# Performance work log

Hardware: AMD Instinct MI355X
Metric: run time of the kernel (lower is better)

Reference implementation:

```python
import jax, jax.numpy as jnp
import numpy as np

H = 1024          # rnn hidden dim
D = H // 2        # coarse/fine half
E = H // 8        # embed dim = 128
COND = H // 2     # conditioning (upsampled mel) dim = 512
EPS = 1e-5
TILE = 16


def _bn(x, scale, offset):
    # haiku BatchNorm, training mode: batch stats over (N, L)
    mean = jnp.mean(x, axis=(0, 1), keepdims=True)
    var = jnp.mean(jnp.square(x), axis=(0, 1), keepdims=True) - jnp.square(mean)
    return scale * (x - mean) * jax.lax.rsqrt(var + EPS) + offset


def _conv(x, w, rate=1):
    return jax.lax.conv_general_dilated(
        x, w, window_strides=(1,), padding='VALID', rhs_dilation=(rate,),
        dimension_numbers=('NWC', 'WIO', 'NWC'))


def _up(x, w, stride):
    # Conv1DTranspose with kernel 1, SAME padding: scatter x@w to positions i*stride
    N, L, _ = x.shape
    y = jnp.einsum('nlc,cd->nld', x, w)
    out = jnp.zeros((N, L, stride, y.shape[-1]), y.dtype).at[:, :, 0, :].set(y)
    return out.reshape(N, L * stride, y.shape[-1])


def _iw_mask():
    m = jnp.ones((COND + 3 * E, 3 * H), jnp.float32)
    for j in (0, 2, 4):  # coarse_t embed cannot see coarse half of u, r, e gates
        m = m.at[-E:, j * D:(j + 1) * D].set(0.0)
    return m


def _forward(x, mel, conv_in_w, bn0_s, bn0_o, dconv1_w, bn1_s, bn1_o,
             dconv2_w, bn2_s, bn2_o, up1_w, bn3_s, bn3_o, up2_w, bn4_s, bn4_o,
             up3_w, bn5_s, bn5_o, I_W, I_b, R_w, R_b,
             O1_w, O1_b, O2_w, O2_b, O3_w, O3_b, O4_w, O4_b, c_embed, f_embed):
    # ---- UpsampleNetwork ----
    h = jax.nn.relu(_bn(_conv(mel, conv_in_w), bn0_s, bn0_o))
    r1 = jax.nn.relu(_bn(_conv(h, dconv1_w, rate=2), bn1_s, bn1_o))
    h = h[:, 1:-1] + r1
    r2 = jax.nn.relu(_bn(_conv(h, dconv2_w, rate=4), bn2_s, bn2_o))
    h = h[:, 2:-2] + r2
    h = jax.nn.relu(_bn(_up(h, up1_w, 2), bn3_s, bn3_o))
    h = jax.nn.relu(_bn(_up(h, up2_w, 2), bn4_s, bn4_o))
    h = jax.nn.relu(_bn(_up(h, up3_w, 4), bn5_s, bn5_o))
    N, Lm, Dm = h.shape
    mel_up = jnp.tile(h[:, :, None, :], (1, 1, TILE, 1)).reshape(N, Lm * TILE, Dm)

    # ---- WaveRNNOriginal.__call__ (teacher-forced GRU) ----
    coarse, fine, coarse_t = x[..., 0], x[..., 1], x[..., 2]
    inputs = jnp.concatenate(
        (mel_up, c_embed[coarse], f_embed[fine], c_embed[coarse_t]), axis=-1)
    # precompute input projection for all timesteps  [N, L, 3H]
    ix = jnp.einsum('nli,ij->nlj', inputs, I_W * _iw_mask()) + I_b.reshape(1, 1, -1)
    ix_t = jnp.swapaxes(ix, 0, 1)  # time-major [L, N, 3H]
    h0 = jnp.zeros((N, H), ix.dtype)

    def step(hx, xt):
        u1, r1_, e1 = jnp.split(hx @ R_w + R_b, 3, axis=-1)
        u2, r2_, e2 = jnp.split(xt, 3, axis=-1)
        ut = jax.nn.sigmoid(u1 + u2)
        rt = jax.nn.sigmoid(r1_ + r2_)
        et = jnp.tanh(rt * e1 + e2)
        ht = ut * hx + (1.0 - ut) * et
        return ht, ht

    _, hs = jax.lax.scan(step, h0, ix_t)
    hs = jnp.swapaxes(hs, 0, 1)              # [N, L, H]
    yc, yf = jnp.split(hs, 2, axis=-1)       # [N, L, H/2] each
    clog = jax.nn.relu(yc @ O1_w + O1_b) @ O2_w + O2_b
    flog = jax.nn.relu(yf @ O3_w + O3_b) @ O4_w + O4_b
    logits = jnp.stack((clog, flog), axis=-1)  # [N, L, 256, 2]
    return jax.nn.log_softmax(logits, axis=-2)


def setup_inputs():
    key = jax.random.key(0)
    ks = jax.random.split(key, 24)
    n = jax.random.normal
    N, T = 2, 24
    L = (T - 8) * 256  # 4096
    inp = {
        'x': jax.random.randint(ks[0], (N, L, 3), 0, 256),
        'mel': n(ks[1], (N, T, 80), jnp.float32),
        'conv_in_w': n(ks[2], (3, 80, 512)) * 0.05,
        'dconv1_w': n(ks[3], (2, 512, 512)) * 0.05,
        'dconv2_w': n(ks[4], (2, 512, 512)) * 0.05,
        'up1_w': n(ks[5], (512, 512)) * 0.05,
        'up2_w': n(ks[6], (512, 512)) * 0.05,
        'up3_w': n(ks[7], (512, COND)) * 0.05,
        'I_W': n(ks[8], (COND + 3 * E, 3 * H)) * 0.03,
        'I_b': jnp.zeros((3 * H,)),
        'R_w': n(ks[9], (H, 3 * H)) * 0.03,
        'R_b': jnp.zeros((3 * H,)),
        'O1_w': n(ks[10], (D, D)) * 0.05,
        'O1_b': jnp.zeros((D,)),
        'O2_w': n(ks[11], (D, 256)) * 0.05,
        'O2_b': jnp.zeros((256,)),
        'O3_w': n(ks[12], (D, D)) * 0.05,
        'O3_b': jnp.zeros((D,)),
        'O4_w': n(ks[13], (D, 256)) * 0.05,
        'O4_b': jnp.zeros((256,)),
        'c_embed': n(ks[14], (256, E)) * 0.1,
        'f_embed': n(ks[15], (256, E)) * 0.1,
    }
    for i in range(6):
        c = COND if i == 5 else 512
        inp[f'bn{i}_s'] = jnp.ones((c,))
        inp[f'bn{i}_o'] = jnp.zeros((c,))
    return inp


def reference(x, mel, conv_in_w, dconv1_w, dconv2_w, up1_w, up2_w, up3_w,
              I_W, I_b, R_w, R_b, O1_w, O1_b, O2_w, O2_b, O3_w, O3_b,
              O4_w, O4_b, c_embed, f_embed,
              bn0_s, bn0_o, bn1_s, bn1_o, bn2_s, bn2_o,
              bn3_s, bn3_o, bn4_s, bn4_o, bn5_s, bn5_o):
    return _forward(x, mel, conv_in_w, bn0_s, bn0_o, dconv1_w, bn1_s, bn1_o,
                    dconv2_w, bn2_s, bn2_o, up1_w, bn3_s, bn3_o, up2_w, bn4_s,
                    bn4_o, up3_w, bn5_s, bn5_o, I_W, I_b, R_w, R_b,
                    O1_w, O1_b, O2_w, O2_b, O3_w, O3_b, O4_w, O4_b,
                    c_embed, f_embed)
```

## Files before the change

kernel.cpp:

```cpp
#include <hip/hip_runtime.h>
#include <hip/hip_bf16.h>
#include <math.h>

__device__ __forceinline__ float bf2f(unsigned short u) {
  unsigned int x = ((unsigned int)u) << 16;
  return __builtin_bit_cast(float, x);
}
__device__ __forceinline__ float lo16(unsigned int u) {
  return __builtin_bit_cast(float, u << 16);
}
__device__ __forceinline__ float hi16(unsigned int u) {
  return __builtin_bit_cast(float, u & 0xffff0000u);
}
__device__ __forceinline__ unsigned short f2bf(float f) {
  unsigned int x = __builtin_bit_cast(unsigned int, f);
  unsigned int lsb = (x >> 16) & 1u;
  x += 0x7fffu + lsb;
  return (unsigned short)(x >> 16);
}
template <bool BF>
__device__ __forceinline__ float ld(const void* p, size_t i) {
  if (BF) return bf2f(((const unsigned short*)p)[i]);
  return ((const float*)p)[i];
}

#define SCOPE_AGENT __HIP_MEMORY_SCOPE_AGENT
typedef unsigned long long ull;

__global__ void k_init(const unsigned int* bn0s, ull* sbuf, int* dt) {
  int t = threadIdx.x;
  for (int i = t; i < 4096; i += 256) sbuf[i] = 0ULL;
  if (t == 0) dt[0] = (bn0s[0] == 0x3F803F80u) ? 1 : 0;
}

template <bool BF>
__device__ void conv_in_body(const void* mel, const void* w, float* out) {
  int idx = blockIdx.x * 256 + threadIdx.x;
  if (idx >= 2 * 22 * 512) return;
  int c = idx & 511, l = (idx >> 9) % 22, n = idx / (22 * 512);
  float acc = 0.f;
  for (int kw = 0; kw < 3; kw++) {
    size_t mrow = (size_t)(n * 24 + l + kw) * 80;
    size_t wrow = (size_t)kw * 80 * 512 + c;
#pragma unroll 4
    for (int i = 0; i < 80; i++)
      acc += ld<BF>(mel, mrow + i) * ld<BF>(w, wrow + (size_t)i * 512);
  }
  out[idx] = acc;
}
__global__ void k_conv_in(const void* mel, const void* w, float* out, const int* dt) {
  if (dt[0]) conv_in_body<true>(mel, w, out); else conv_in_body<false>(mel, w, out);
}

template <bool BF>
__device__ void dconv_body(const float* in, const void* w, float* out,
                           int Lin, int Lout, int rate) {
  int idx = blockIdx.x * 256 + threadIdx.x;
  if (idx >= 2 * Lout * 512) return;
  int c = idx & 511, l = (idx >> 9) % Lout, n = idx / (Lout * 512);
  float acc = 0.f;
  for (int kw = 0; kw < 2; kw++) {
    const float* irow = in + (n * Lin + l + kw * rate) * 512;
    size_t wrow = (size_t)kw * 512 * 512 + c;
#pragma unroll 4
    for (int i = 0; i < 512; i++)
      acc += irow[i] * ld<BF>(w, wrow + (size_t)i * 512);
  }
  out[idx] = acc;
}
__global__ void k_dconv(const float* in, const void* w, float* out,
                        int Lin, int Lout, int rate, const int* dt) {
  if (dt[0]) dconv_body<true>(in, w, out, Lin, Lout, rate);
  else dconv_body<false>(in, w, out, Lin, Lout, rate);
}

template <bool BF>
__device__ void up_body(const float* in, const void* w, float* out, int Lin, int stride) {
  int Lout = Lin * stride;
  int idx = blockIdx.x * 256 + threadIdx.x;
  if (idx >= 2 * Lout * 512) return;
  int c = idx & 511, lo = (idx >> 9) % Lout, n = idx / (Lout * 512);
  if (lo % stride) { out[idx] = 0.f; return; }
  const float* irow = in + (n * Lin + lo / stride) * 512;
  float acc = 0.f;
#pragma unroll 4
  for (int i = 0; i < 512; i++) acc += irow[i] * ld<BF>(w, (size_t)i * 512 + c);
  out[idx] = acc;
}
__global__ void k_up(const float* in, const void* w, float* out,
                     int Lin, int stride, const int* dt) {
  if (dt[0]) up_body<true>(in, w, out, Lin, stride);
  else up_body<false>(in, w, out, Lin, stride);
}

__global__ void k_bnstats(const float* __restrict__ x, float* __restrict__ st, int NL) {
  int c = blockIdx.x * 256 + threadIdx.x;
  if (c >= 512) return;
  float s = 0.f, s2 = 0.f;
  for (int r = 0; r < NL; r++) { float v = x[r * 512 + c]; s += v; s2 += v * v; }
  float m = s / (float)NL;
  float var = s2 / (float)NL - m * m;
  st[c] = m;
  st[512 + c] = rsqrtf(var + 1e-5f);
}

template <bool BF>
__device__ void bnrelu_body(const float* x, float* y, const float* st,
                            const void* sc, const void* of,
                            const float* res, int resL, int shift, int L) {
  int idx = blockIdx.x * 256 + threadIdx.x;
  if (idx >= 2 * L * 512) return;
  int c = idx & 511, l = (idx >> 9) % L, n = idx / (L * 512);
  float v = (x[idx] - st[c]) * st[512 + c] * ld<BF>(sc, c) + ld<BF>(of, c);
  v = fmaxf(v, 0.f);
  if (res) v += res[(n * resL + l + shift) * 512 + c];
  y[idx] = v;
}
__global__ void k_bnrelu(const float* x, float* y, const float* st,
                         const void* sc, const void* of,
                         const float* res, int resL, int shift, int L, const int* dt) {
  if (dt[0]) bnrelu_body<true>(x, y, st, sc, of, res, resL, shift, L);
  else bnrelu_body<false>(x, y, st, sc, of, res, resL, shift, L);
}

template <bool BF>
__device__ void M_body(const float* h5, const void* IW, const void* Ib,
                       const void* Rb, float* M, float* hl) {
  int bid = blockIdx.x;
  int rt = bid / 12, ct = bid % 12;
  int r0 = rt * 8, j = ct * 256 + threadIdx.x;
  const float4* src = (const float4*)(h5 + (size_t)r0 * 512);
  float4* dst = (float4*)hl;
  for (int q = threadIdx.x; q < 1024; q += 256) dst[q] = src[q];
  __syncthreads();
  float acc[8];
#pragma unroll
  for (int r = 0; r < 8; r++) acc[r] = 0.f;
  for (int k = 0; k < 512; k += 4) {
    float w0 = ld<BF>(IW, (size_t)k * 3072 + j);
    float w1 = ld<BF>(IW, (size_t)(k + 1) * 3072 + j);
    float w2 = ld<BF>(IW, (size_t)(k + 2) * 3072 + j);
    float w3 = ld<BF>(IW, (size_t)(k + 3) * 3072 + j);
#pragma unroll
    for (int r = 0; r < 8; r++) {
      float4 h4 = *(const float4*)(hl + r * 512 + k);
      acc[r] += h4.x * w0 + h4.y * w1 + h4.z * w2 + h4.w * w3;
    }
  }
  float bias = ld<BF>(Ib, j) + ((j < 2048) ? ld<BF>(Rb, j) : 0.f);
#pragma unroll
  for (int r = 0; r < 8; r++) M[(size_t)(r0 + r) * 3072 + j] = acc[r] + bias;
}
__global__ __launch_bounds__(256) void k_M(const float* h5, const void* IW,
                                           const void* Ib, const void* Rb,
                                           float* M, const int* dt) {
  __shared__ float hl[8 * 512];
  if (dt[0]) M_body<true>(h5, IW, Ib, Rb, M, hl);
  else M_body<false>(h5, IW, Ib, Rb, M, hl);
}

template <bool BF>
__device__ void T_body(const void* emb, const void* IW, int row0, int maskcoarse,
                       float* T, float* el) {
  int bid = blockIdx.x;
  int vt = bid / 12, ct = bid % 12;
  int v0 = vt * 8, j = ct * 256 + threadIdx.x;
  for (int q = threadIdx.x; q < 1024; q += 256)
    el[q] = ld<BF>(emb, (size_t)v0 * 128 + q);
  __syncthreads();
  float acc[8];
#pragma unroll
  for (int r = 0; r < 8; r++) acc[r] = 0.f;
  for (int k = 0; k < 128; k += 4) {
    float w0 = ld<BF>(IW, (size_t)(row0 + k) * 3072 + j);
    float w1 = ld<BF>(IW, (size_t)(row0 + k + 1) * 3072 + j);
    float w2 = ld<BF>(IW, (size_t)(row0 + k + 2) * 3072 + j);
    float w3 = ld<BF>(IW, (size_t)(row0 + k + 3) * 3072 + j);
#pragma unroll
    for (int r = 0; r < 8; r++) {
      float4 e4 = *(const float4*)(el + r * 128 + k);
      acc[r] += e4.x * w0 + e4.y * w1 + e4.z * w2 + e4.w * w3;
    }
  }
  bool mask = maskcoarse && ((j & 1023) < 512);
#pragma unroll
  for (int r = 0; r < 8; r++)
    T[(size_t)(v0 + r) * 3072 + j] = mask ? 0.f : acc[r];
}
__global__ __launch_bounds__(256) void k_T(const void* emb, const void* IW, int row0,
                                           int maskcoarse, float* T, const int* dt) {
  __shared__ float el[8 * 128];
  if (dt[0]) T_body<true>(emb, IW, row0, maskcoarse, T, el);
  else T_body<false>(emb, IW, row0, maskcoarse, T, el);
}

#define NWG 128
template <bool BF>
__device__ void gru_body(const float* __restrict__ M, const float* __restrict__ T1,
                         const float* __restrict__ T2, const float* __restrict__ T3,
                         const int* __restrict__ x, const void* Rw, const void* Rb,
                         ull* sbuf, unsigned short* __restrict__ hs, float* hlds) {
  const int g = blockIdx.x, tid = threadIdx.x;
  const int n = g >> 6;
  const int il = tid >> 5, ks = tid & 31;
  const int i = (g & 63) * 16 + il;
  const int koff = ks * 32;
  const int k0 = tid * 2;
  const int lidx = (k0 >> 6) * 68 + (k0 & 63);

  float wreg[96];
#pragma unroll
  for (int gt = 0; gt < 3; gt++)
#pragma unroll
    for (int kk = 0; kk < 32; kk++)
      wreg[gt * 32 + kk] = ld<BF>(Rw, (size_t)(koff + kk) * 3072 + gt * 1024 + i);
  const float rbe = ld<BF>(Rb, 2048 + i);

  float hprev = 0.f;

  for (int t = 0; t < 4096; t++) {
    float* hb = hlds + (t & 1) * (16 * 68);

    float au = 0.f, ar = 0.f, ae = 0.f;
    if (ks == 0) {
      const int* xr = x + (n * 4096 + t) * 3;
      int ci = xr[0], fi = xr[1], cti = xr[2];
      const float* mr = M + (size_t)(n * 256 + (t >> 4)) * 3072;
      const float* p1 = T1 + (size_t)ci * 3072;
      const float* p2 = T2 + (size_t)fi * 3072;
      const float* p3 = T3 + (size_t)cti * 3072;
      au = mr[i] + p1[i] + p2[i] + p3[i];
      ar = mr[1024 + i] + p1[1024 + i] + p2[1024 + i] + p3[1024 + i];
      ae = mr[2048 + i] + p1[2048 + i] + p2[2048 + i] + p3[2048 + i];
    }

    const ull thr = (ull)(unsigned int)t << 32;
    ull* sb = sbuf + (size_t)(((t & 1) << 1) + n) * 1024 + k0;
    ull s0, s1;
    while (true) {
      s0 = __hip_atomic_load(sb + 0, __ATOMIC_RELAXED, SCOPE_AGENT);
      s1 = __hip_atomic_load(sb + 1, __ATOMIC_RELAXED, SCOPE_AGENT);
      if (s0 >= thr && s1 >= thr) break;
    }
    float2 h2;
    h2.x = __builtin_bit_cast(float, (unsigned int)s0);
    h2.y = __builtin_bit_cast(float, (unsigned int)s1);
    *(float2*)(hb + lidx) = h2;
    __syncthreads();

    float du = 0.f, dr = 0.f, de = 0.f;
    const float* hp = hb + (ks >> 1) * 68 + (ks & 1) * 32;
#pragma unroll
    for (int kk = 0; kk < 32; kk += 4) {
      float4 h4 = *(const float4*)(hp + kk);
      du += wreg[kk] * h4.x + wreg[kk + 1] * h4.y + wreg[kk + 2] * h4.z + wreg[kk + 3] * h4.w;
      dr += wreg[32 + kk] * h4.x + wreg[33 + kk] * h4.y + wreg[34 + kk] * h4.z + wreg[35 + kk] * h4.w;
      de += wreg[64 + kk] * h4.x + wreg[65 + kk] * h4.y + wreg[66 + kk] * h4.z + wreg[67 + kk] * h4.w;
    }
#pragma unroll
    for (int off = 16; off > 0; off >>= 1) {
      du += __shfl_xor(du, off, 32);
      dr += __shfl_xor(dr, off, 32);
      de += __shfl_xor(de, off, 32);
    }

    if (ks == 0) {
      float u = 1.f / (1.f + __expf(-(du + au)));
      float r = 1.f / (1.f + __expf(-(dr + ar)));
      float w = r * (de + rbe) + ae;
      float e = 1.f - 2.f / (__expf(2.f * w) + 1.f);
      float ht = u * hprev + (1.f - u) * e;
      hprev = ht;
      ull slot = ((ull)(unsigned int)(t + 1) << 32) |
                 (ull)__builtin_bit_cast(unsigned int, ht);
      __hip_atomic_store(
          sbuf + (size_t)((((t + 1) & 1) << 1) + n) * 1024 + i, slot,
          __ATOMIC_RELAXED, SCOPE_AGENT);
      hs[(size_t)(n * 4096 + t) * 1024 + i] = f2bf(ht);
    }
  }
}
__global__ __launch_bounds__(512, 1) void k_gru(
    const float* M, const float* T1, const float* T2, const float* T3,
    const int* x, const void* Rw, const void* Rb,
    ull* sbuf, unsigned short* hs, const int* dt) {
  __shared__ __align__(16) float hlds[2 * 16 * 68];
  if (dt[0]) gru_body<true>(M, T1, T2, T3, x, Rw, Rb, sbuf, hs, hlds);
  else gru_body<false>(M, T1, T2, T3, x, Rw, Rb, sbuf, hs, hlds);
}

template <bool BF>
__device__ void out1_body(const unsigned short* __restrict__ hs,
                          const void* O1w, const void* O1b,
                          const void* O3w, const void* O3b,
                          unsigned short* __restrict__ tmid, unsigned short* lds) {
  int b = blockIdx.x, tid = threadIdx.x;
  size_t r0 = (size_t)b * 16;
  const uint4* src = (const uint4*)(hs + r0 * 1024);
  uint4* dst = (uint4*)lds;
  for (int q = tid; q < 2048; q += 256) dst[q] = src[q];
  __syncthreads();
  const unsigned int* lds32 = (const unsigned int*)lds;

  float acc[4][16];
#pragma unroll
  for (int jg = 0; jg < 4; jg++)
#pragma unroll
    for (int r = 0; r < 16; r++) acc[jg][r] = 0.f;

  for (int k = 0; k < 512; k += 2) {
    float w0a = ld<BF>(O1w, (size_t)k * 512 + tid);
    float w1a = ld<BF>(O1w, (size_t)k * 512 + 256 + tid);
    float w2a = ld<BF>(O3w, (size_t)k * 512 + tid);
    float w3a = ld<BF>(O3w, (size_t)k * 512 + 256 + tid);
    float w0b = ld<BF>(O1w, (size_t)(k + 1) * 512 + tid);
    float w1b = ld<BF>(O1w, (size_t)(k + 1) * 512 + 256 + tid);
    float w2b = ld<BF>(O3w, (size_t)(k + 1) * 512 + tid);
    float w3b = ld<BF>(O3w, (size_t)(k + 1) * 512 + 256 + tid);
#pragma unroll
    for (int r = 0; r < 16; r++) {
      unsigned int pc = lds32[r * 512 + (k >> 1)];
      unsigned int pf = lds32[r * 512 + 256 + (k >> 1)];
      float hc0 = lo16(pc), hc1 = hi16(pc);
      float hf0 = lo16(pf), hf1 = hi16(pf);
      acc[0][r] += hc0 * w0a + hc1 * w0b;
      acc[1][r] += hc0 * w1a + hc1 * w1b;
      acc[2][r] += hf0 * w2a + hf1 * w2b;
      acc[3][r] += hf0 * w3a + hf1 * w3b;
    }
  }
  float bia[4] = { ld<BF>(O1b, tid), ld<BF>(O1b, 256 + tid),
                   ld<BF>(O3b, tid), ld<BF>(O3b, 256 + tid) };
#pragma unroll
  for (int jg = 0; jg < 4; jg++)
#pragma unroll
    for (int r = 0; r < 16; r++) {
      float v = fmaxf(acc[jg][r] + bia[jg], 0.f);
      tmid[(r0 + r) * 1024 + jg * 256 + tid] = f2bf(v);
    }
}
__global__ __launch_bounds__(256) void k_out1(
    const unsigned short* hs, const void* O1w, const void* O1b,
    const void* O3w, const void* O3b, unsigned short* tmid, const int* dt) {
  __shared__ unsigned short lds[16 * 1024];
  if (dt[0]) out1_body<true>(hs, O1w, O1b, O3w, O3b, tmid, lds);
  else out1_body<false>(hs, O1w, O1b, O3w, O3b, tmid, lds);
}

__device__ __forceinline__ float blkmax(float v, float* red, int tid) {
#pragma unroll
  for (int off = 32; off > 0; off >>= 1) v = fmaxf(v, __shfl_xor(v, off));
  __syncthreads();
  if ((tid & 63) == 0) red[tid >> 6] = v;
  __syncthreads();
  return fmaxf(fmaxf(red[0], red[1]), fmaxf(red[2], red[3]));
}
__device__ __forceinline__ float blksum(float v, float* red, int tid) {
#pragma unroll
  for (int off = 32; off > 0; off >>= 1) v += __shfl_xor(v, off);
  __syncthreads();
  if ((tid & 63) == 0) red[tid >> 6] = v;
  __syncthreads();
  return red[0] + red[1] + red[2] + red[3];
}

template <bool BF>
__device__ void out2_body(const unsigned short* __restrict__ tmid,
                          const void* O2w, const void* O2b,
                          const void* O4w, const void* O4b,
                          void* out, unsigned short* lds, float* red) {
  int b = blockIdx.x, tid = threadIdx.x, q = tid;
  size_t r0 = (size_t)b * 16;
  const uint4* src = (const uint4*)(tmid + r0 * 1024);
  uint4* dst = (uint4*)lds;
  for (int p = tid; p < 2048; p += 256) dst[p] = src[p];
  __syncthreads();
  const unsigned int* lds32 = (const unsigned int*)lds;

  float ac[16], af[16];
#pragma unroll
  for (int r = 0; r < 16; r++) { ac[r] = 0.f; af[r] = 0.f; }
  for (int j = 0; j < 512; j += 2) {
    float w2a = ld<BF>(O2w, (size_t)j * 256 + q);
    float w4a = ld<BF>(O4w, (size_t)j * 256 + q);
    float w2b = ld<BF>(O2w, (size_t)(j + 1) * 256 + q);
    float w4b = ld<BF>(O4w, (size_t)(j + 1) * 256 + q);
#pragma unroll
    for (int r = 0; r < 16; r++) {
      unsigned int pc = lds32[r * 512 + (j >> 1)];
      unsigned int pf = lds32[r * 512 + 256 + (j >> 1)];
      ac[r] += lo16(pc) * w2a + hi16(pc) * w2b;
      af[r] += lo16(pf) * w4a + hi16(pf) * w4b;
    }
  }
  float b2 = ld<BF>(O2b, q), b4 = ld<BF>(O4b, q);
  for (int r = 0; r < 16; r++) {
    float c = ac[r] + b2;
    float f = af[r] + b4;
    float mc = blkmax(c, red, tid);
    float sc = blksum(__expf(c - mc), red, tid);
    float mf = blkmax(f, red, tid);
    float sf = blksum(__expf(f - mf), red, tid);
    size_t row = r0 + r;
    float oc = c - mc - logf(sc);
    float of_ = f - mf - logf(sf);
    if (BF) {
      ((unsigned short*)out)[(row * 256 + q) * 2 + 0] = f2bf(oc);
      ((unsigned short*)out)[(row * 256 + q) * 2 + 1] = f2bf(of_);
    } else {
      ((float*)out)[(row * 256 + q) * 2 + 0] = oc;
      ((float*)out)[(row * 256 + q) * 2 + 1] = of_;
    }
  }
}
__global__ __launch_bounds__(256) void k_out2(
    const unsigned short* tmid, const void* O2w, const void* O2b,
    const void* O4w, const void* O4b, void* out, const int* dt) {
  __shared__ unsigned short lds[16 * 1024];
  __shared__ float red[8];
  if (dt[0]) out2_body<true>(tmid, O2w, O2b, O4w, O4b, out, lds, red);
  else out2_body<false>(tmid, O2w, O2b, O4w, O4b, out, lds, red);
}

extern "C" void kernel_launch(void* const* d_in, const int* in_sizes, int n_in,
                              void* d_out, int out_size, void* d_ws, size_t ws_size,
                              hipStream_t stream) {
  const int* x = (const int*)d_in[0];
  const void* mel = d_in[1];
  const void* conv_in_w = d_in[2];
  const void* dconv1_w = d_in[3];
  const void* dconv2_w = d_in[4];
  const void* up1_w = d_in[5];
  const void* up2_w = d_in[6];
  const void* up3_w = d_in[7];
  const void* IW = d_in[8];
  const void* Ib = d_in[9];
  const void* Rw = d_in[10];
  const void* Rb = d_in[11];
  const void* O1w = d_in[12];
  const void* O1b = d_in[13];
  const void* O2w = d_in[14];
  const void* O2b = d_in[15];
  const void* O3w = d_in[16];
  const void* O3b = d_in[17];
  const void* O4w = d_in[18];
  const void* O4b = d_in[19];
  const void* c_embed = d_in[20];
  const void* f_embed = d_in[21];
  const void* bns[6], *bno[6];
  for (int s = 0; s < 6; s++) {
    bns[s] = d_in[22 + 2 * s];
    bno[s] = d_in[23 + 2 * s];
  }

  float* ws = (float*)d_ws;
  float* A = ws;
  float* B = A + 262144;
  float* st = B + 262144;
  float* M = st + 1024;
  float* T1 = M + 1572864;
  float* T2 = T1 + 786432;
  float* T3 = T2 + 786432;
  ull* sbuf = (ull*)(T3 + 786432);
  int* dt = (int*)(sbuf + 4096);
  unsigned short* hs = (unsigned short*)(dt + 4);
  unsigned short* tmid = hs + 8388608;

  k_init<<<1, 256, 0, stream>>>((const unsigned int*)bns[0], sbuf, dt);

  k_conv_in<<<88, 256, 0, stream>>>(mel, conv_in_w, A, dt);
  k_bnstats<<<2, 256, 0, stream>>>(A, st, 44);
  k_bnrelu<<<88, 256, 0, stream>>>(A, A, st, bns[0], bno[0], nullptr, 0, 0, 22, dt);

  k_dconv<<<80, 256, 0, stream>>>(A, dconv1_w, B, 22, 20, 2, dt);
  k_bnstats<<<2, 256, 0, stream>>>(B, st, 40);
  k_bnrelu<<<80, 256, 0, stream>>>(B, B, st, bns[1], bno[1], A, 22, 1, 20, dt);

  k_dconv<<<64, 256, 0, stream>>>(B, dconv2_w, A, 20, 16, 4, dt);
  k_bnstats<<<2, 256, 0, stream>>>(A, st, 32);
  k_bnrelu<<<64, 256, 0, stream>>>(A, A, st, bns[2], bno[2], B, 20, 2, 16, dt);

  k_up<<<128, 256, 0, stream>>>(A, up1_w, B, 16, 2, dt);
  k_bnstats<<<2, 256, 0, stream>>>(B, st, 64);
  k_bnrelu<<<128, 256, 0, stream>>>(B, B, st, bns[3], bno[3], nullptr, 0, 0, 32, dt);

  k_up<<<256, 256, 0, stream>>>(B, up2_w, A, 32, 2, dt);
  k_bnstats<<<2, 256, 0, stream>>>(A, st, 128);
  k_bnrelu<<<256, 256, 0, stream>>>(A, A, st, bns[4], bno[4], nullptr, 0, 0, 64, dt);

  k_up<<<1024, 256, 0, stream>>>(A, up3_w, B, 64, 4, dt);
  k_bnstats<<<2, 256, 0, stream>>>(B, st, 512);
  k_bnrelu<<<1024, 256, 0, stream>>>(B, B, st, bns[5], bno[5], nullptr, 0, 0, 256, dt);

  k_M<<<768, 256, 0, stream>>>(B, IW, Ib, Rb, M, dt);
  k_T<<<384, 256, 0, stream>>>(c_embed, IW, 512, 0, T1, dt);
  k_T<<<384, 256, 0, stream>>>(f_embed, IW, 640, 0, T2, dt);
  k_T<<<384, 256, 0, stream>>>(c_embed, IW, 768, 1, T3, dt);

  k_gru<<<NWG, 512, 0, stream>>>(M, T1, T2, T3, x, Rw, Rb, sbuf, hs, dt);

  k_out1<<<512, 256, 0, stream>>>(hs, O1w, O1b, O3w, O3b, tmid, dt);
  k_out2<<<512, 256, 0, stream>>>(tmid, O2w, O2b, O4w, O4b, d_out, dt);

  (void)in_sizes; (void)n_in; (void)out_size; (void)ws_size;
}
```

Measured before the change: 9.082 ms.

## Fuse output MLP stages and parallelize batchnorm statistics across wavefronts

The two output kernels are merged into one, so the intermediate ReLU activations stay in shared memory and are no longer written to and re-read from global memory. The softmax reductions for the coarse and fine heads now share barriers, which cuts the number of block synchronizations per row. Separately, the batchnorm statistics kernel now gives each channel its own wavefront and reduces with shuffles, launching 128 blocks instead of 2. The fused kernel uses twice the shared memory per block, which may lower occupancy.

```diff
diff --git a/kernel.cpp b/kernel.cpp
--- a/kernel.cpp
+++ b/kernel.cpp
@@ -93,15 +93,25 @@
   else up_body<false>(in, w, out, Lin, stride);
 }
 
-__global__ void k_bnstats(const float* __restrict__ x, float* __restrict__ st, int NL) {
-  int c = blockIdx.x * 256 + threadIdx.x;
-  if (c >= 512) return;
+__global__ __launch_bounds__(256) void k_bnstats(const float* __restrict__ x,
+                                                 float* __restrict__ st, int NL) {
+  int c = blockIdx.x * 4 + (threadIdx.x >> 6);
+  int lane = threadIdx.x & 63;
   float s = 0.f, s2 = 0.f;
-  for (int r = 0; r < NL; r++) { float v = x[r * 512 + c]; s += v; s2 += v * v; }
-  float m = s / (float)NL;
-  float var = s2 / (float)NL - m * m;
-  st[c] = m;
-  st[512 + c] = rsqrtf(var + 1e-5f);
+  for (int r = lane; r < NL; r += 64) {
+    float v = x[r * 512 + c];
+    s += v; s2 += v * v;
+  }
+#pragma unroll
+  for (int off = 32; off > 0; off >>= 1) {
+    s += __shfl_xor(s, off);
+    s2 += __shfl_xor(s2, off);
+  }
+  if (lane == 0) {
+    float m = s / (float)NL;
+    st[c] = m;
+    st[512 + c] = rsqrtf(s2 / (float)NL - m * m + 1e-5f);
+  }
 }
 
 template <bool BF>
@@ -290,17 +300,19 @@
 }
 
 template <bool BF>
-__device__ void out1_body(const unsigned short* __restrict__ hs,
-                          const void* O1w, const void* O1b,
-                          const void* O3w, const void* O3b,
-                          unsigned short* __restrict__ tmid, unsigned short* lds) {
+__device__ void out_body(const unsigned short* __restrict__ hs,
+                         const void* O1w, const void* O1b,
+                         const void* O3w, const void* O3b,
+                         const void* O2w, const void* O2b,
+                         const void* O4w, const void* O4b,
+                         void* out, unsigned short* ldsh, unsigned short* ldst) {
   int b = blockIdx.x, tid = threadIdx.x;
   size_t r0 = (size_t)b * 16;
   const uint4* src = (const uint4*)(hs + r0 * 1024);
-  uint4* dst = (uint4*)lds;
+  uint4* dst = (uint4*)ldsh;
   for (int q = tid; q < 2048; q += 256) dst[q] = src[q];
   __syncthreads();
-  const unsigned int* lds32 = (const unsigned int*)lds;
+  const unsigned int* h32 = (const unsigned int*)ldsh;
 
   float acc[4][16];
 #pragma unroll
@@ -319,8 +331,8 @@
     float w3b = ld<BF>(O3w, (size_t)(k + 1) * 512 + 256 + tid);
 #pragma unroll
     for (int r = 0; r < 16; r++) {
-      unsigned int pc = lds32[r * 512 + (k >> 1)];
-      unsigned int pf = lds32[r * 512 + 256 + (k >> 1)];
+      unsigned int pc = h32[r * 512 + (k >> 1)];
+      unsigned int pf = h32[r * 512 + 256 + (k >> 1)];
       float hc0 = lo16(pc), hc1 = hi16(pc);
       float hf0 = lo16(pf), hf1 = hi16(pf);
       acc[0][r] += hc0 * w0a + hc1 * w0b;
@@ -336,90 +348,79 @@
 #pragma unroll
     for (int r = 0; r < 16; r++) {
       float v = fmaxf(acc[jg][r] + bia[jg], 0.f);
-      tmid[(r0 + r) * 1024 + jg * 256 + tid] = f2bf(v);
-    }
-}
-__global__ __launch_bounds__(256) void k_out1(
-    const unsigned short* hs, const void* O1w, const void* O1b,
-    const void* O3w, const void* O3b, unsigned short* tmid, const int* dt) {
-  __shared__ unsigned short lds[16 * 1024];
-  if (dt[0]) out1_body<true>(hs, O1w, O1b, O3w, O3b, tmid, lds);
-  else out1_body<false>(hs, O1w, O1b, O3w, O3b, tmid, lds);
-}
-
-__device__ __forceinline__ float blkmax(float v, float* red, int tid) {
-#pragma unroll
-  for (int off = 32; off > 0; off >>= 1) v = fmaxf(v, __shfl_xor(v, off));
+      ldst[r * 1024 + jg * 256 + tid] = f2bf(v);
+    }
   __syncthreads();
-  if ((tid & 63) == 0) red[tid >> 6] = v;
-  __syncthreads();
-  return fmaxf(fmaxf(red[0], red[1]), fmaxf(red[2], red[3]));
-}
-__device__ __forceinline__ float blksum(float v, float* red, int tid) {
-#pragma unroll
-  for (int off = 32; off > 0; off >>= 1) v += __shfl_xor(v, off);
-  __syncthreads();
-  if ((tid & 63) == 0) red[tid >> 6] = v;
-  __syncthreads();
-  return red[0] + red[1] + red[2] + red[3];
-}
-
-template <bool BF>
-__device__ void out2_body(const unsigned short* __restrict__ tmid,
-                          const void* O2w, const void* O2b,
-                          const void* O4w, const void* O4b,
-                          void* out, unsigned short* lds, float* red) {
-  int b = blockIdx.x, tid = threadIdx.x, q = tid;
-  size_t r0 = (size_t)b * 16;
-  const uint4* src = (const uint4*)(tmid + r0 * 1024);
-  uint4* dst = (uint4*)lds;
-  for (int p = tid; p < 2048; p += 256) dst[p] = src[p];
-  __syncthreads();
-  const unsigned int* lds32 = (const unsigned int*)lds;
+  const unsigned int* t32 = (const unsigned int*)ldst;
 
   float ac[16], af[16];
 #pragma unroll
   for (int r = 0; r < 16; r++) { ac[r] = 0.f; af[r] = 0.f; }
   for (int j = 0; j < 512; j += 2) {
-    float w2a = ld<BF>(O2w, (size_t)j * 256 + q);
-    float w4a = ld<BF>(O4w, (size_t)j * 256 + q);
-    float w2b = ld<BF>(O2w, (size_t)(j + 1) * 256 + q);
-    float w4b = ld<BF>(O4w, (size_t)(j + 1) * 256 + q);
+    float w2a = ld<BF>(O2w, (size_t)j * 256 + tid);
+    float w4a = ld<BF>(O4w, (size_t)j * 256 + tid);
+    float w2b = ld<BF>(O2w, (size_t)(j + 1) * 256 + tid);
+    float w4b = ld<BF>(O4w, (size_t)(j + 1) * 256 + tid);
 #pragma unroll
     for (int r = 0; r < 16; r++) {
-      unsigned int pc = lds32[r * 512 + (j >> 1)];
-      unsigned int pf = lds32[r * 512 + 256 + (j >> 1)];
+      unsigned int pc = t32[r * 512 + (j >> 1)];
+      unsigned int pf = t32[r * 512 + 256 + (j >> 1)];
       ac[r] += lo16(pc) * w2a + hi16(pc) * w2b;
       af[r] += lo16(pf) * w4a + hi16(pf) * w4b;
     }
   }
-  float b2 = ld<BF>(O2b, q), b4 = ld<BF>(O4b, q);
+  float b2 = ld<BF>(O2b, tid), b4 = ld<BF>(O4b, tid);
+
+  __syncthreads();
+  float* red = (float*)ldsh;
   for (int r = 0; r < 16; r++) {
     float c = ac[r] + b2;
     float f = af[r] + b4;
-    float mc = blkmax(c, red, tid);
-    float sc = blksum(__expf(c - mc), red, tid);
-    float mf = blkmax(f, red, tid);
-    float sf = blksum(__expf(f - mf), red, tid);
+    float mc, sc, mf, sf, v;
+    v = c;
+#pragma unroll
+    for (int off = 32; off > 0; off >>= 1) v = fmaxf(v, __shfl_xor(v, off));
+    if ((tid & 63) == 0) red[tid >> 6] = v;
+    v = f;
+#pragma unroll
+    for (int off = 32; off > 0; off >>= 1) v = fmaxf(v, __shfl_xor(v, off));
+    if ((tid & 63) == 0) red[4 + (tid >> 6)] = v;
+    __syncthreads();
+    mc = fmaxf(fmaxf(red[0], red[1]), fmaxf(red[2], red[3]));
+    mf = fmaxf(fmaxf(red[4], red[5]), fmaxf(red[6], red[7]));
+    __syncthreads();
+    v = __expf(c - mc);
+#pragma unroll
+    for (int off = 32; off > 0; off >>= 1) v += __shfl_xor(v, off);
+    if ((tid & 63) == 0) red[tid >> 6] = v;
+    v = __expf(f - mf);
+#pragma unroll
+    for (int off = 32; off > 0; off >>= 1) v += __shfl_xor(v, off);
+    if ((tid & 63) == 0) red[4 + (tid >> 6)] = v;
+    __syncthreads();
+    sc = red[0] + red[1] + red[2] + red[3];
+    sf = red[4] + red[5] + red[6] + red[7];
+    __syncthreads();
     size_t row = r0 + r;
     float oc = c - mc - logf(sc);
     float of_ = f - mf - logf(sf);
     if (BF) {
-      ((unsigned short*)out)[(row * 256 + q) * 2 + 0] = f2bf(oc);
-      ((unsigned short*)out)[(row * 256 + q) * 2 + 1] = f2bf(of_);
+      ((unsigned short*)out)[(row * 256 + tid) * 2 + 0] = f2bf(oc);
+      ((unsigned short*)out)[(row * 256 + tid) * 2 + 1] = f2bf(of_);
     } else {
-      ((float*)out)[(row * 256 + q) * 2 + 0] = oc;
-      ((float*)out)[(row * 256 + q) * 2 + 1] = of_;
-    }
-  }
-}
-__global__ __launch_bounds__(256) void k_out2(
-    const unsigned short* tmid, const void* O2w, const void* O2b,
+      ((float*)out)[(row * 256 + tid) * 2 + 0] = oc;
+      ((float*)out)[(row * 256 + tid) * 2 + 1] = of_;
+    }
+  }
+}
+__global__ __launch_bounds__(256) void k_out(
+    const unsigned short* hs, const void* O1w, const void* O1b,
+    const void* O3w, const void* O3b, const void* O2w, const void* O2b,
     const void* O4w, const void* O4b, void* out, const int* dt) {
-  __shared__ unsigned short lds[16 * 1024];
-  __shared__ float red[8];
-  if (dt[0]) out2_body<true>(tmid, O2w, O2b, O4w, O4b, out, lds, red);
-  else out2_body<false>(tmid, O2w, O2b, O4w, O4b, out, lds, red);
+  __shared__ __align__(16) unsigned short ldsh[16 * 1024];
+  __shared__ __align__(16) unsigned short ldst[16 * 1024];
+  if (dt[0]) out_body<true>(hs, O1w, O1b, O3w, O3b, O2w, O2b, O4w, O4b, out, ldsh, ldst);
+  else out_body<false>(hs, O1w, O1b, O3w, O3b, O2w, O2b, O4w, O4b, out, ldsh, ldst);
 }
 
 extern "C" void kernel_launch(void* const* d_in, const int* in_sizes, int n_in,
@@ -464,32 +465,31 @@
   ull* sbuf = (ull*)(T3 + 786432);
   int* dt = (int*)(sbuf + 4096);
   unsigned short* hs = (unsigned short*)(dt + 4);
-  unsigned short* tmid = hs + 8388608;
 
   k_init<<<1, 256, 0, stream>>>((const unsigned int*)bns[0], sbuf, dt);
 
   k_conv_in<<<88, 256, 0, stream>>>(mel, conv_in_w, A, dt);
-  k_bnstats<<<2, 256, 0, stream>>>(A, st, 44);
+  k_bnstats<<<128, 256, 0, stream>>>(A, st, 44);
   k_bnrelu<<<88, 256, 0, stream>>>(A, A, st, bns[0], bno[0], nullptr, 0, 0, 22, dt);
 
   k_dconv<<<80, 256, 0, stream>>>(A, dconv1_w, B, 22, 20, 2, dt);
-  k_bnstats<<<2, 256, 0, stream>>>(B, st, 40);
+  k_bnstats<<<128, 256, 0, stream>>>(B, st, 40);
   k_bnrelu<<<80, 256, 0, stream>>>(B, B, st, bns[1], bno[1], A, 22, 1, 20, dt);
 
   k_dconv<<<64, 256, 0, stream>>>(B, dconv2_w, A, 20, 16, 4, dt);
-  k_bnstats<<<2, 256, 0, stream>>>(A, st, 32);
+  k_bnstats<<<128, 256, 0, stream>>>(A, st, 32);
   k_bnrelu<<<64, 256, 0, stream>>>(A, A, st, bns[2], bno[2], B, 20, 2, 16, dt);
 
   k_up<<<128, 256, 0, stream>>>(A, up1_w, B, 16, 2, dt);
-  k_bnstats<<<2, 256, 0, stream>>>(B, st, 64);
+  k_bnstats<<<128, 256, 0, stream>>>(B, st, 64);
   k_bnrelu<<<128, 256, 0, stream>>>(B, B, st, bns[3], bno[3], nullptr, 0, 0, 32, dt);
 
   k_up<<<256, 256, 0, stream>>>(B, up2_w, A, 32, 2, dt);
-  k_bnstats<<<2, 256, 0, stream>>>(A, st, 128);
+  k_bnstats<<<128, 256, 0, stream>>>(A, st, 128);
   k_bnrelu<<<256, 256, 0, stream>>>(A, A, st, bns[4], bno[4], nullptr, 0, 0, 64, dt);
 
   k_up<<<1024, 256, 0, stream>>>(A, up3_w, B, 64, 4, dt);
-  k_bnstats<<<2, 256, 0, stream>>>(B, st, 512);
+  k_bnstats<<<128, 256, 0, stream>>>(B, st, 512);
   k_bnrelu<<<1024, 256, 0, stream>>>(B, B, st, bns[5], bno[5], nullptr, 0, 0, 256, dt);
 
   k_M<<<768, 256, 0, stream>>>(B, IW, Ib, Rb, M, dt);
@@ -499,8 +499,8 @@
 
   k_gru<<<NWG, 512, 0, stream>>>(M, T1, T2, T3, x, Rw, Rb, sbuf, hs, dt);
 
-  k_out1<<<512, 256, 0, stream>>>(hs, O1w, O1b, O3w, O3b, tmid, dt);
-  k_out2<<<512, 256, 0, stream>>>(tmid, O2w, O2b, O4w, O4b, d_out, dt);
+  k_out<<<512, 256, 0, stream>>>(hs, O1w, O1b, O3w, O3b, O2w, O2b, O4w, O4b,
+                                 d_out, dt);
 
   (void)in_sizes; (void)n_in; (void)out_size; (void)ws_size;
 }
```

Result: no change. 9.029 ms (-0.6%).
